# Kernel tuning notes

Hardware: AMD Instinct MI355X
Metric: run time of the kernel (lower is better)

## Reference

```python
import jax, jax.numpy as jnp
import numpy as np

T, B, H, I = 128, 128, 256, 256


def setup_inputs() -> dict:
    key = jax.random.key(0)
    ks = jax.random.split(key, 8)
    s = 1.0 / np.sqrt(H)
    embs = jax.random.normal(ks[0], (T, B, I), jnp.float32)
    # lens in [1, T] (a length of 0 is meaningless for this module)
    lens = jnp.maximum(jax.random.randint(ks[1], (B,), 0, T + 1), 1)
    Wih = jax.random.uniform(ks[2], (4 * H, I), jnp.float32, -s, s)
    Whh = jax.random.uniform(ks[3], (4 * H, H), jnp.float32, -s, s)
    bih = jax.random.uniform(ks[4], (4 * H,), jnp.float32, -s, s)
    bhh = jax.random.uniform(ks[5], (4 * H,), jnp.float32, -s, s)
    Wa = jax.random.uniform(ks[6], (H, 2 * H), jnp.float32, -s, s)
    ba = jnp.zeros((H,), jnp.float32)
    return {"embs": embs, "lens": lens, "Wih": Wih, "Whh": Whh,
            "bih": bih, "bhh": bhh, "Wa": Wa, "ba": ba}


def _forward(embs, Wih, Whh, bih, bhh, Wa, ba):
    Tn, Bn, _ = embs.shape
    Hn = Whh.shape[1]
    h0 = jnp.zeros((Bn, Hn), embs.dtype)
    c0 = jnp.zeros((Bn, Hn), embs.dtype)
    hids0 = jnp.zeros((Tn, Bn, Hn), embs.dtype)  # growing history of outputs
    pos = jnp.arange(Tn)

    def step(carry, emb):
        h, c, hids, t = carry
        # attention of current hidden over all previous outputs (dot-product scores)
        scores = jnp.einsum('bh,tbh->tb', h, hids)          # [T,B]
        valid = pos[:, None] < jnp.maximum(t, 1)             # at least one valid slot avoids NaN
        scores = jnp.where(valid, scores, -1e30)
        w = jax.nn.softmax(scores, axis=0)
        ctx = jnp.einsum('tb,tbh->bh', w, hids)              # [B,H]
        h_att = jnp.tanh(jnp.concatenate([h, ctx], axis=-1) @ Wa.T + ba)
        h_in = jnp.where(t > 0, h_att, h)                    # no attention before first output
        # one LSTM cell step (PyTorch gate order: i, f, g, o)
        gates = emb @ Wih.T + bih + h_in @ Whh.T + bhh       # [B,4H]
        i, f, g, o = jnp.split(gates, 4, axis=-1)
        c_new = jax.nn.sigmoid(f) * c + jax.nn.sigmoid(i) * jnp.tanh(g)
        h_new = jax.nn.sigmoid(o) * jnp.tanh(c_new)
        hids = jax.lax.dynamic_update_slice(hids, h_new[None], (t, 0, 0))
        return (h_new, c_new, hids, t + 1), (h_new, c_new)

    _, (hs, cs) = jax.lax.scan(step, (h0, c0, hids0, jnp.int32(0)), embs)
    return hs, cs  # each [T,B,H]


def reference(embs, lens, Wih, Whh, bih, bhh, Wa, ba):
    hs, cs = _forward(embs, Wih, Whh, bih, bhh, Wa, ba)
    bidx = jnp.arange(hs.shape[1])
    h_fin = hs[lens - 1, bidx][None]  # [1,B,H], state at t == len-1
    c_fin = cs[lens - 1, bidx][None]
    return hs, h_fin, c_fin
```

## Files before the change

kernel.cpp:

```cpp
#include <hip/hip_runtime.h>
#include <math.h>

#define T 128
#define B 128
#define H 256
#define I 256
#define G4 1024
#define NB 2

typedef unsigned short u16;
typedef unsigned int u32;
typedef _Float16 half_t;
typedef _Float16 half2_t __attribute__((ext_vector_type(2)));

#if defined(__has_builtin)
#if __has_builtin(__builtin_amdgcn_fdot2)
#define HAS_FDOT2 1
#endif
#endif

__device__ __forceinline__ float fdot2(half2_t a, half2_t b, float c) {
#ifdef HAS_FDOT2
    return __builtin_amdgcn_fdot2(a, b, c, false);
#else
    return fmaf((float)a.x, (float)b.x, fmaf((float)a.y, (float)b.y, c));
#endif
}
__device__ __forceinline__ half2_t h2cast(u32 u) { return __builtin_bit_cast(half2_t, u); }

__device__ __forceinline__ float sigmoid_fast(float x) {
    return 1.0f / (1.0f + __expf(-x));
}
__device__ __forceinline__ float tanh_fast(float x) {
    x = fminf(fmaxf(x, -15.f), 15.f);
    const float e = __expf(2.0f * x);
    return (e - 1.0f) / (e + 1.0f);
}

#define BARL() do {                                        \
    asm volatile("s_waitcnt lgkmcnt(0)" ::: "memory");     \
    __builtin_amdgcn_s_barrier();                          \
} while (0)

__global__ void pack_whH(const float* __restrict__ Whh, half2_t* __restrict__ WhH) {
    const int k2 = blockIdx.x;
    const int o  = threadIdx.x;
    half2_t v;
    v.x = (half_t)Whh[(size_t)o * H + 2 * k2];
    v.y = (half_t)Whh[(size_t)o * H + 2 * k2 + 1];
    WhH[(size_t)k2 * G4 + o] = v;
}
__global__ void pack_waH(const float* __restrict__ Wa, half2_t* __restrict__ WaH) {
    const int k2 = blockIdx.x;
    const int j  = threadIdx.x;
    half2_t v;
    v.x = (half_t)Wa[(size_t)j * (2 * H) + 2 * k2];
    v.y = (half_t)Wa[(size_t)j * (2 * H) + 2 * k2 + 1];
    WaH[(size_t)k2 * H + j] = v;
}

__global__ __launch_bounds__(256) void gemm_g(const float* __restrict__ A,
                                              const float* __restrict__ W,
                                              const float* __restrict__ bih,
                                              const float* __restrict__ bhh,
                                              float* __restrict__ G) {
    __shared__ __align__(16) float As[64][68];
    __shared__ __align__(16) float Ws[64][68];
    const int m0 = blockIdx.x * 64;
    const int n0 = blockIdx.y * 64;
    const int tid = threadIdx.x;
    const int ty = tid >> 4, tx = tid & 15;
    const int rr = tid >> 4;
    const int kr = tid & 15;

    float acc[4][4] = {};
    for (int k0 = 0; k0 < I; k0 += 64) {
#pragma unroll
        for (int i = 0; i < 4; ++i) {
            const int r = rr + 16 * i;
            const float4 av = *(const float4*)&A[(size_t)(m0 + r) * I + k0 + kr * 4];
            const float4 wv = *(const float4*)&W[(size_t)(n0 + r) * I + k0 + kr * 4];
            As[kr * 4 + 0][r] = av.x; As[kr * 4 + 1][r] = av.y;
            As[kr * 4 + 2][r] = av.z; As[kr * 4 + 3][r] = av.w;
            Ws[kr * 4 + 0][r] = wv.x; Ws[kr * 4 + 1][r] = wv.y;
            Ws[kr * 4 + 2][r] = wv.z; Ws[kr * 4 + 3][r] = wv.w;
        }
        __syncthreads();
#pragma unroll 8
        for (int kk = 0; kk < 64; ++kk) {
            const float4 a4 = *(const float4*)&As[kk][ty * 4];
            const float4 w4 = *(const float4*)&Ws[kk][tx * 4];
            const float a[4] = {a4.x, a4.y, a4.z, a4.w};
            const float w[4] = {w4.x, w4.y, w4.z, w4.w};
#pragma unroll
            for (int i = 0; i < 4; ++i)
#pragma unroll
                for (int jj = 0; jj < 4; ++jj)
                    acc[i][jj] = fmaf(a[i], w[jj], acc[i][jj]);
        }
        __syncthreads();
    }
    const int n = n0 + tx * 4;
    const float4 bi = *(const float4*)&bih[n];
    const float4 bh = *(const float4*)&bhh[n];
    const float4 bb = make_float4(bi.x + bh.x, bi.y + bh.y, bi.z + bh.z, bi.w + bh.w);
#pragma unroll
    for (int i = 0; i < 4; ++i) {
        const int m = m0 + ty * 4 + i;
        float4 o = make_float4(acc[i][0] + bb.x, acc[i][1] + bb.y,
                               acc[i][2] + bb.z, acc[i][3] + bb.w);
        *(float4*)&G[(size_t)m * G4 + n] = o;
    }
}

__global__ __launch_bounds__(1024, 4) void alstm7(
    const int* __restrict__ lens,
    const float* __restrict__ G,
    const half2_t* __restrict__ WhH,
    const half2_t* __restrict__ WaH,
    const float* __restrict__ ba,
    float* __restrict__ out)
{
    __shared__ __align__(16) half_t hid_s[NB][T][H];
    __shared__ __align__(16) float  sc_s[NB][T];
    __shared__ __align__(16) half_t hH_s[NB][H];
    __shared__ __align__(16) half_t hcI_s[4 * 256];
    __shared__ __align__(16) half_t hinI_s[4 * 128];
    __shared__ __align__(16) float  red_s[2048];
    __shared__ __align__(16) float  gate_s[NB][G4];

    const int b0 = blockIdx.x * NB;
    const int tid = threadIdx.x;
    const int lane = tid & 63;
    const int wave = tid >> 6;
    const int sb = wave >> 3;
    const int stp0 = wave & 7;
    const int cb = tid >> 9;
    const int ck = (tid >> 8) & 1;
    const int cj = tid & 255;
    const int ako = tid >> 8;
    const int aj = tid & 255;
    const int eb = tid >> 8;
    const int ej = tid & 255;

    const int len0 = lens[b0], len1 = lens[b0 + 1];
    float c_reg = 0.f;
    float* hfin = out + (size_t)T * B * H;
    float* cfin = hfin + (size_t)B * H;
    if (tid < 512) hH_s[eb][ej] = (half_t)0.f;
    BARL();

    for (int t = 0; t < T; ++t) {
        const float gA = G[((size_t)t * B + b0) * G4 + tid];
        const float gB = G[((size_t)t * B + b0 + 1) * G4 + tid];

        if (t > 0) {
            {
                const half2_t h2a = h2cast(*(const u32*)&hH_s[sb][lane * 4]);
                const half2_t h2b = h2cast(*(const u32*)&hH_s[sb][lane * 4 + 2]);
                for (int tp = stp0; tp < t; tp += 8) {
                    const uint2 hv = *(const uint2*)&hid_s[sb][tp][lane * 4];
                    float d = fdot2(h2cast(hv.x), h2a, fdot2(h2cast(hv.y), h2b, 0.f));
#pragma unroll
                    for (int off = 32; off; off >>= 1) d += __shfl_xor(d, off);
                    if (lane == 0) sc_s[sb][tp] = d;
                }
            }
            BARL();
            if (stp0 == 0) {
                const float v0 = (lane < t) ? sc_s[sb][lane] : -3.0e38f;
                const float v1 = (lane + 64 < t) ? sc_s[sb][lane + 64] : -3.0e38f;
                float m = fmaxf(v0, v1);
#pragma unroll
                for (int off = 32; off; off >>= 1) m = fmaxf(m, __shfl_xor(m, off));
                const float e0 = (lane < t) ? __expf(v0 - m) : 0.f;
                const float e1 = (lane + 64 < t) ? __expf(v1 - m) : 0.f;
                float s = e0 + e1;
#pragma unroll
                for (int off = 32; off; off >>= 1) s += __shfl_xor(s, off);
                const float inv = 1.f / s;
                if (lane < t) sc_s[sb][lane] = e0 * inv;
                if (lane + 64 < t) sc_s[sb][lane + 64] = e1 * inv;
            }
            BARL();
            {
                float cacc = 0.f;
                for (int tp = ck; tp < t; tp += 2)
                    cacc = fmaf(sc_s[cb][tp], (float)hid_s[cb][tp][cj], cacc);
                red_s[cb * 512 + ck * 256 + cj] = cacc;
                gate_s[0][tid] = gA;
                gate_s[1][tid] = gB;
            }
            BARL();
            if (tid < 512) {
                const float ctxv = red_s[eb * 512 + ej] + red_s[eb * 512 + 256 + ej];
                hcI_s[512 + 4 * (ej >> 1) + 2 * eb + (ej & 1)] = (half_t)ctxv;
            }
            BARL();
            {
                const half2_t* wp = &WaH[(size_t)(ako * 64) * H + aj];
                float a0 = 0.f, a1 = 0.f;
#pragma unroll 8
                for (int kk = 0; kk < 64; ++kk) {
                    const int k2 = ako * 64 + kk;
                    const uint2 hh = *(const uint2*)&hcI_s[4 * k2];
                    const half2_t w = wp[(size_t)kk * H];
                    a0 = fdot2(w, h2cast(hh.x), a0);
                    a1 = fdot2(w, h2cast(hh.y), a1);
                }
                red_s[ako * 512 + aj] = a0;
                red_s[ako * 512 + 256 + aj] = a1;
            }
            BARL();
            if (tid < 512) {
                float a = ba[ej];
#pragma unroll
                for (int r = 0; r < 4; ++r) a += red_s[r * 512 + eb * 256 + ej];
                hinI_s[4 * (ej >> 1) + 2 * eb + (ej & 1)] = (half_t)tanh_fast(a);
            }
            BARL();
            {
                const half2_t* wp = &WhH[tid];
                float g0 = 0.f, g1 = 0.f;
#pragma unroll 8
                for (int k2 = 0; k2 < 128; ++k2) {
                    const uint2 hh = *(const uint2*)&hinI_s[4 * k2];
                    const half2_t w = wp[(size_t)k2 * G4];
                    g0 = fdot2(w, h2cast(hh.x), g0);
                    g1 = fdot2(w, h2cast(hh.y), g1);
                }
                red_s[tid] = g0;
                red_s[1024 + tid] = g1;
            }
        } else {
            gate_s[0][tid] = gA;
            gate_s[1][tid] = gB;
            red_s[tid] = 0.f;
            red_s[1024 + tid] = 0.f;
        }
        BARL();
        if (tid < 512) {
            const int bg = b0 + eb;
            const float gi = gate_s[eb][ej]         + red_s[eb * 1024 + ej];
            const float gf = gate_s[eb][H + ej]     + red_s[eb * 1024 + H + ej];
            const float gg = gate_s[eb][2 * H + ej] + red_s[eb * 1024 + 2 * H + ej];
            const float go = gate_s[eb][3 * H + ej] + red_s[eb * 1024 + 3 * H + ej];
            const float ig = sigmoid_fast(gi);
            const float fg = sigmoid_fast(gf);
            const float gv = tanh_fast(gg);
            const float og = sigmoid_fast(go);
            c_reg = fmaf(fg, c_reg, ig * gv);
            const float h_new = og * tanh_fast(c_reg);
            const half_t hh = (half_t)h_new;
            hH_s[eb][ej] = hh;
            hid_s[eb][t][ej] = hh;
            hcI_s[4 * (ej >> 1) + 2 * eb + (ej & 1)] = hh;
            out[((size_t)t * B + bg) * H + ej] = h_new;
            const int lb = eb ? len1 : len0;
            if (t == lb - 1) {
                hfin[(size_t)bg * H + ej] = h_new;
                cfin[(size_t)bg * H + ej] = c_reg;
            }
        }
        BARL();
    }
}

extern "C" void kernel_launch(void* const* d_in, const int* in_sizes, int n_in,
                              void* d_out, int out_size, void* d_ws, size_t ws_size,
                              hipStream_t stream) {
    const float* embs = (const float*)d_in[0];
    const int*   lens = (const int*)d_in[1];
    const float* Wih  = (const float*)d_in[2];
    const float* Whh  = (const float*)d_in[3];
    const float* bih  = (const float*)d_in[4];
    const float* bhh  = (const float*)d_in[5];
    const float* Wa   = (const float*)d_in[6];
    const float* ba   = (const float*)d_in[7];
    float* out = (float*)d_out;

    float* G      = (float*)d_ws;
    half2_t* WhH  = (half2_t*)(G + (size_t)T * B * G4);
    half2_t* WaH  = WhH + (size_t)128 * G4;

    pack_whH<<<128, G4, 0, stream>>>(Whh, WhH);
    pack_waH<<<256, H, 0, stream>>>(Wa, WaH);
    dim3 ggrid(T * B / 64, G4 / 64);
    gemm_g<<<ggrid, 256, 0, stream>>>(embs, Wih, bih, bhh, G);
    alstm7<<<B / NB, 1024, 0, stream>>>(lens, G, WhH, WaH, ba, out);
}
```

Before: 1.891 ms.

## Fuse softmax into context accumulation and overlap Wa h-half with ctx reduction

Every wave now recomputes the softmax max and sum redundantly, and the context accumulation uses unnormalized exponentials. Normalization is deferred to the context reduction through a shared inverse sum, which removes one barrier and the separate normalization pass. The Wa matvec is split so the h-half (threads 512+) runs while threads below 512 reduce the context, and the ctx-half runs after. The cost is redundant exp evaluations per element, plus a doubled reduction buffer and pointer hoisting for weights.

After: 2.034 ms. +7.5%, slower.

```diff
diff --git a/kernel.cpp b/kernel.cpp
--- a/kernel.cpp
+++ b/kernel.cpp
@@ -113,7 +113,7 @@
     }
 }
 
-__global__ __launch_bounds__(1024, 4) void alstm7(
+__global__ __launch_bounds__(1024, 4) void alstm9(
     const int* __restrict__ lens,
     const float* __restrict__ G,
     const half2_t* __restrict__ WhH,
@@ -127,7 +127,9 @@
     __shared__ __align__(16) half_t hcI_s[4 * 256];
     __shared__ __align__(16) half_t hinI_s[4 * 128];
     __shared__ __align__(16) float  red_s[2048];
+    __shared__ __align__(16) float  wa_red[2048];
     __shared__ __align__(16) float  gate_s[NB][G4];
+    __shared__            float  invs_s[2];
 
     const int b0 = blockIdx.x * NB;
     const int tid = threadIdx.x;
@@ -138,8 +140,9 @@
     const int cb = tid >> 9;
     const int ck = (tid >> 8) & 1;
     const int cj = tid & 255;
-    const int ako = tid >> 8;
     const int aj = tid & 255;
+    const int akoh = (tid >> 8) - 2;
+    const int akoc = (tid >> 8) + 2;
     const int eb = tid >> 8;
     const int ej = tid & 255;
 
@@ -148,6 +151,10 @@
     float* hfin = out + (size_t)T * B * H;
     float* cfin = hfin + (size_t)B * H;
     if (tid < 512) hH_s[eb][ej] = (half_t)0.f;
+
+    const half2_t* wph = (tid >= 512) ? &WaH[(size_t)(akoh * 64) * H + aj] : WaH;
+    const half2_t* wpc = (tid < 512)  ? &WaH[(size_t)(akoc * 64) * H + aj] : WaH;
+    const half2_t* whp = &WhH[tid];
     BARL();
 
     for (int t = 0; t < T; ++t) {
@@ -167,65 +174,72 @@
                 }
             }
             BARL();
-            if (stp0 == 0) {
-                const float v0 = (lane < t) ? sc_s[sb][lane] : -3.0e38f;
-                const float v1 = (lane + 64 < t) ? sc_s[sb][lane + 64] : -3.0e38f;
+            {
+                const float v0 = (lane < t) ? sc_s[cb][lane] : -3.0e38f;
+                const float v1 = (lane + 64 < t) ? sc_s[cb][lane + 64] : -3.0e38f;
                 float m = fmaxf(v0, v1);
 #pragma unroll
                 for (int off = 32; off; off >>= 1) m = fmaxf(m, __shfl_xor(m, off));
-                const float e0 = (lane < t) ? __expf(v0 - m) : 0.f;
-                const float e1 = (lane + 64 < t) ? __expf(v1 - m) : 0.f;
-                float s = e0 + e1;
+                float s = ((lane < t) ? __expf(v0 - m) : 0.f)
+                        + ((lane + 64 < t) ? __expf(v1 - m) : 0.f);
 #pragma unroll
                 for (int off = 32; off; off >>= 1) s += __shfl_xor(s, off);
-                const float inv = 1.f / s;
-                if (lane < t) sc_s[sb][lane] = e0 * inv;
-                if (lane + 64 < t) sc_s[sb][lane + 64] = e1 * inv;
-            }
-            BARL();
-            {
+                if (lane == 0 && (wave == 0 || wave == 8)) invs_s[cb] = 1.f / s;
                 float cacc = 0.f;
-                for (int tp = ck; tp < t; tp += 2)
-                    cacc = fmaf(sc_s[cb][tp], (float)hid_s[cb][tp][cj], cacc);
+                for (int tp = ck; tp < t; tp += 2) {
+                    const float e = __expf(sc_s[cb][tp] - m);
+                    cacc = fmaf(e, (float)hid_s[cb][tp][cj], cacc);
+                }
                 red_s[cb * 512 + ck * 256 + cj] = cacc;
                 gate_s[0][tid] = gA;
                 gate_s[1][tid] = gB;
             }
             BARL();
             if (tid < 512) {
-                const float ctxv = red_s[eb * 512 + ej] + red_s[eb * 512 + 256 + ej];
+                const float invs = invs_s[eb];
+                const float ctxv = (red_s[eb * 512 + ej] + red_s[eb * 512 + 256 + ej]) * invs;
                 hcI_s[512 + 4 * (ej >> 1) + 2 * eb + (ej & 1)] = (half_t)ctxv;
-            }
-            BARL();
-            {
-                const half2_t* wp = &WaH[(size_t)(ako * 64) * H + aj];
+            } else {
                 float a0 = 0.f, a1 = 0.f;
 #pragma unroll 8
                 for (int kk = 0; kk < 64; ++kk) {
-                    const int k2 = ako * 64 + kk;
+                    const int k2 = akoh * 64 + kk;
                     const uint2 hh = *(const uint2*)&hcI_s[4 * k2];
-                    const half2_t w = wp[(size_t)kk * H];
+                    const half2_t w = wph[(size_t)kk * H];
                     a0 = fdot2(w, h2cast(hh.x), a0);
                     a1 = fdot2(w, h2cast(hh.y), a1);
                 }
-                red_s[ako * 512 + aj] = a0;
-                red_s[ako * 512 + 256 + aj] = a1;
+                wa_red[akoh * 512 + aj] = a0;
+                wa_red[akoh * 512 + 256 + aj] = a1;
+            }
+            BARL();
+            if (tid < 512) {
+                float a0 = 0.f, a1 = 0.f;
+#pragma unroll 8
+                for (int kk = 0; kk < 64; ++kk) {
+                    const int k2 = akoc * 64 + kk;
+                    const uint2 hh = *(const uint2*)&hcI_s[4 * k2];
+                    const half2_t w = wpc[(size_t)kk * H];
+                    a0 = fdot2(w, h2cast(hh.x), a0);
+                    a1 = fdot2(w, h2cast(hh.y), a1);
+                }
+                wa_red[akoc * 512 + aj] = a0;
+                wa_red[akoc * 512 + 256 + aj] = a1;
             }
             BARL();
             if (tid < 512) {
                 float a = ba[ej];
 #pragma unroll
-                for (int r = 0; r < 4; ++r) a += red_s[r * 512 + eb * 256 + ej];
+                for (int r = 0; r < 4; ++r) a += wa_red[r * 512 + eb * 256 + ej];
                 hinI_s[4 * (ej >> 1) + 2 * eb + (ej & 1)] = (half_t)tanh_fast(a);
             }
             BARL();
             {
-                const half2_t* wp = &WhH[tid];
                 float g0 = 0.f, g1 = 0.f;
 #pragma unroll 8
                 for (int k2 = 0; k2 < 128; ++k2) {
                     const uint2 hh = *(const uint2*)&hinI_s[4 * k2];
-                    const half2_t w = wp[(size_t)k2 * G4];
+                    const half2_t w = whp[(size_t)k2 * G4];
                     g0 = fdot2(w, h2cast(hh.x), g0);
                     g1 = fdot2(w, h2cast(hh.y), g1);
                 }
@@ -287,5 +301,5 @@
     pack_waH<<<256, H, 0, stream>>>(Wa, WaH);
     dim3 ggrid(T * B / 64, G4 / 64);
     gemm_g<<<ggrid, 256, 0, stream>>>(embs, Wih, bih, bhh, G);
-    alstm7<<<B / NB, 1024, 0, stream>>>(lens, G, WhH, WaH, ba, out);
-}
+    alstm9<<<B / NB, 1024, 0, stream>>>(lens, G, WhH, WaH, ba, out);
+}
```
